# Kernel optimization log

Measured on AMD Instinct MI355X. Metric: run time of the kernel, lower is better.

Reference implementation:

```python
import jax, jax.numpy as jnp
import numpy as np
import math

NB_HEADS = 16
NUM_BUCKETS = 32
MAX_DISTANCE = 128


def _rel_bucket(qlen, klen, num_buckets=NUM_BUCKETS, max_distance=MAX_DISTANCE):
    # static (numpy) computation of T5 relative-position buckets, bidirectional
    relpos = np.arange(qlen)[:, None] - np.arange(klen)[None, :]
    n = -relpos
    nb = num_buckets // 2
    ret = (n < 0).astype(np.int64) * nb
    n = np.abs(n)
    max_exact = nb // 2
    is_small = n < max_exact
    val_if_large = max_exact + (
        np.log(np.maximum(n, 1) / max_exact) / math.log(max_distance / max_exact) * (nb - max_exact)
    ).astype(np.int64)
    val_if_large = np.minimum(val_if_large, nb - 1)
    return ret + np.where(is_small, n, val_if_large)


def _layer_normalize(x):
    # faithful to source: mean/biased-std over last dim, NO epsilon, no affine
    m = jnp.mean(x, axis=-1, keepdims=True)
    var = jnp.mean((x - m) ** 2, axis=-1, keepdims=True)
    return (x - m) / jnp.sqrt(var)


def setup_inputs() -> dict:
    key = jax.random.key(0)
    ks = jax.random.split(key, 16)
    B, L, D, F = 4, 1024, 1024, 4096
    s = 0.02
    inp = {
        "x": jax.random.normal(ks[0], (B, L, D), jnp.float32),
        "padding_mask": jnp.ones((B, L), jnp.int32),
        "Wq": jax.random.normal(ks[1], (D, D), jnp.float32) * s,
        "bq": jnp.zeros((D,), jnp.float32),
        "Wk": jax.random.normal(ks[2], (D, D), jnp.float32) * s,
        "bk": jnp.zeros((D,), jnp.float32),
        "Wv": jax.random.normal(ks[3], (D, D), jnp.float32) * s,
        "bv": jnp.zeros((D,), jnp.float32),
        "Wo": jax.random.normal(ks[4], (D, D), jnp.float32) * s,
        "bo": jnp.zeros((D,), jnp.float32),
        "rel_emb": jax.random.normal(ks[5], (NUM_BUCKETS, NB_HEADS), jnp.float32) * s,
        "W1": jax.random.normal(ks[6], (F, D), jnp.float32) * s,
        "b1": jnp.zeros((F,), jnp.float32),
        "W2": jax.random.normal(ks[7], (D, F), jnp.float32) * s,
        "b2": jnp.zeros((D,), jnp.float32),
    }
    return inp


def reference(x, padding_mask, Wq, bq, Wk, bk, Wv, bv, Wo, bo, rel_emb, W1, b1, W2, b2):
    B, L, D = x.shape
    H = NB_HEADS
    dh = D // H

    q = x @ Wq.T + bq
    k = x @ Wk.T + bk
    v = x @ Wv.T + bv

    # NOTE: source does a RAW reshape (B, L, H*dh) -> (B*H, L, dh); reproduce exactly
    qm = q.reshape(B * H, L, dh)
    km = k.reshape(B * H, L, dh)
    vm = v.reshape(B * H, L, dh)

    scores = jnp.einsum("bqd,bkd->bqk", qm, km)  # (B*H, L, L), no 1/sqrt(dh) scaling in source

    # relative position bias: emb[bucket] -> (L, L, H), tile heads B times, permute
    buckets = jnp.asarray(_rel_bucket(L, L))
    pos = rel_emb[buckets]                      # (L, L, H)
    bias = jnp.transpose(jnp.tile(pos, (1, 1, B)), (2, 0, 1))  # (H*B, L, L)
    scores = scores + bias

    # padding mask in log space, tiled exactly like source's repeat+view
    pm = jnp.log(padding_mask.astype(jnp.float32))            # (B, L)
    mask = jnp.tile(pm[:, None, :], (1, L, H)).reshape(-1, L, L)  # (B*H, L, L)
    scores = scores + mask

    p = jax.nn.softmax(scores, axis=-1)  # dropout is identity at p=0 / eval
    att = (p @ vm).reshape(B, L, D)
    att = att @ Wo.T + bo

    att_out = _layer_normalize(att + x)
    ff = jax.nn.relu(att_out @ W1.T + b1) @ W2.T + b2
    ff_out = _layer_normalize(ff + att_out)
    return ff_out
```

## Files before the change

### kernel.cpp

```cpp
#include <hip/hip_runtime.h>
#include <hip/hip_bf16.h>

typedef __hip_bfloat16 bf16;
typedef __attribute__((ext_vector_type(8))) short s8v;
typedef __attribute__((ext_vector_type(4))) float f32x4;

__device__ __forceinline__ float bits2f(unsigned short u) {
    return __uint_as_float(((unsigned)u) << 16);
}
__device__ __forceinline__ unsigned short f2b(float f) {
    union { float f; unsigned u; } x{f};
    return (unsigned short)((x.u + 0x7fff + ((x.u >> 16) & 1)) >> 16);
}
__device__ __forceinline__ float to_f(float x) { return x; }
__device__ __forceinline__ float to_f(unsigned short x) { return bits2f(x); }

__device__ __forceinline__ void load4(const float* p, float* a) {
    float4 t = *(const float4*)p;
    a[0] = t.x; a[1] = t.y; a[2] = t.z; a[3] = t.w;
}
__device__ __forceinline__ void load4(const unsigned short* p, float* a) {
    ushort4 t = *(const ushort4*)p;
    a[0] = bits2f(t.x); a[1] = bits2f(t.y); a[2] = bits2f(t.z); a[3] = bits2f(t.w);
}

__global__ __launch_bounds__(256)
void cvt_all_kernel(const float* __restrict__ x,
                    const float* __restrict__ Wq, const float* __restrict__ Wk,
                    const float* __restrict__ Wv, const float* __restrict__ Wo,
                    const float* __restrict__ W1, const float* __restrict__ W2,
                    unsigned short* __restrict__ xb, unsigned short* __restrict__ Wqkvb,
                    unsigned short* __restrict__ Wob,
                    unsigned short* __restrict__ W1b, unsigned short* __restrict__ W2b)
{
    int i = blockIdx.x * 256 + threadIdx.x;
    const float* src; unsigned short* dst; int off;
    if (i < (1 << 20))      { src = x;  dst = xb;  off = i; }
    else if (i < (2 << 20)) { src = W1; dst = W1b; off = i - (1 << 20); }
    else if (i < (3 << 20)) { src = W2; dst = W2b; off = i - (2 << 20); }
    else {
        int j = i - (3 << 20);
        int sel = j >> 18;
        off = j & ((1 << 18) - 1);
        src = sel == 0 ? Wq : sel == 1 ? Wk : sel == 2 ? Wv : Wo;
        dst = sel == 3 ? Wob : Wqkvb + ((size_t)sel << 20);
    }
    float4 v = ((const float4*)src)[off];
    ushort4 o = { f2b(v.x), f2b(v.y), f2b(v.z), f2b(v.w) };
    ((ushort4*)dst)[off] = o;
}

__global__ void rbias_kernel(const float* __restrict__ rel_emb, unsigned short* __restrict__ rbias)
{
    int idx = blockIdx.x * 256 + threadIdx.x;
    if (idx >= 16 * 2048) return;
    int h = idx >> 11, q = idx & 2047;
    int n = q - 1023, ret = 0;
    if (n < 0) { ret = 16; n = -n; }
    int b;
    if (n < 8) b = n;
    else {
        double t = log((double)n / 8.0) / log(16.0) * 8.0;
        int v = 8 + (int)t;
        b = v < 15 ? v : 15;
    }
    rbias[idx] = f2b(rel_emb[(ret + b) * 16 + h]);
}

template<typename TC, typename TR, int RELU, int QKV>
__global__ __launch_bounds__(256)
void mfma_gemm(const unsigned short* __restrict__ A, int lda,
               const unsigned short* __restrict__ W, int ldw,
               const float* __restrict__ b0, const float* __restrict__ b1,
               const float* __restrict__ b2,
               const TR* __restrict__ res,
               void* __restrict__ C0, void* __restrict__ C1, void* __restrict__ C2,
               int ldc, int M, int N, int Ksplit)
{
    __shared__ unsigned short sm[2 * 128 * 32];
    unsigned short* As = sm;
    unsigned short* Ws = sm + 128 * 32;

    const int tid = threadIdx.x;
    const int w = tid >> 6, lane = tid & 63;
    const int quad = lane >> 4, col = lane & 15;
    const int m0 = blockIdx.y * 128, n0 = blockIdx.x * 128;
    const int wrow = (w & 1) * 64, wcol = (w >> 1) * 64;
    const int kz = blockIdx.z * Ksplit;

    const int srow   = lane >> 2;
    const int schunk = (lane & 3) ^ ((lane >> 4) & 3);

    f32x4 acc[4][4] = {};

    for (int k0 = kz; k0 < kz + Ksplit; k0 += 32) {
        __syncthreads();
        #pragma unroll
        for (int t = 0; t < 2; ++t) {
            const int rbase = w * 32 + t * 16;
            unsigned off = (unsigned)(rbase * 64);
            off = __builtin_amdgcn_readfirstlane(off);
            const unsigned short* ga = A + (size_t)(m0 + rbase + srow) * lda + k0 + schunk * 8;
            __builtin_amdgcn_global_load_lds(
                (const __attribute__((address_space(1))) unsigned int*)ga,
                (__attribute__((address_space(3))) unsigned int*)((char*)As + off), 16, 0, 0);
            const unsigned short* gw = W + (size_t)(n0 + rbase + srow) * ldw + k0 + schunk * 8;
            __builtin_amdgcn_global_load_lds(
                (const __attribute__((address_space(1))) unsigned int*)gw,
                (__attribute__((address_space(3))) unsigned int*)((char*)Ws + off), 16, 0, 0);
        }
        __syncthreads();

        s8v af[4], bfr[4];
        #pragma unroll
        for (int mt = 0; mt < 4; ++mt) {
            int rr = wrow + mt * 16 + col;
            af[mt] = *(const s8v*)(As + rr * 32 + ((quad ^ ((rr >> 2) & 3)) * 8));
        }
        #pragma unroll
        for (int nt = 0; nt < 4; ++nt) {
            int rr = wcol + nt * 16 + col;
            bfr[nt] = *(const s8v*)(Ws + rr * 32 + ((quad ^ ((rr >> 2) & 3)) * 8));
        }
        #pragma unroll
        for (int mt = 0; mt < 4; ++mt)
            #pragma unroll
            for (int nt = 0; nt < 4; ++nt)
                acc[mt][nt] = __builtin_amdgcn_mfma_f32_16x16x32_bf16(af[mt], bfr[nt], acc[mt][nt], 0, 0, 0);
    }

    if (QKV) {
        const int sel = n0 >> 10;
        unsigned short* Cb = (unsigned short*)(sel == 0 ? C0 : sel == 1 ? C1 : C2);
        const float* bs = sel == 0 ? b0 : sel == 1 ? b1 : b2;
        #pragma unroll
        for (int mt = 0; mt < 4; ++mt)
            #pragma unroll
            for (int rg = 0; rg < 4; ++rg) {
                int gm = m0 + wrow + mt * 16 + quad * 4 + rg;
                #pragma unroll
                for (int nt = 0; nt < 4; ++nt) {
                    int gnc = (n0 + wcol + nt * 16 + col) & 1023;
                    Cb[(size_t)gm * 1024 + gnc] = f2b(acc[mt][nt][rg] + bs[gnc]);
                }
            }
    } else {
        void* Cv = blockIdx.z ? C1 : C0;
        const bool z0 = (blockIdx.z == 0);
        #pragma unroll
        for (int mt = 0; mt < 4; ++mt)
            #pragma unroll
            for (int rg = 0; rg < 4; ++rg) {
                int gm = m0 + wrow + mt * 16 + quad * 4 + rg;
                #pragma unroll
                for (int nt = 0; nt < 4; ++nt) {
                    int gn = n0 + wcol + nt * 16 + col;
                    float c = acc[mt][nt][rg];
                    if (z0) {
                        if (b0)  c += b0[gn];
                        if (res) c += to_f(res[(size_t)gm * ldc + gn]);
                    }
                    if (RELU) c = fmaxf(c, 0.f);
                    if (sizeof(TC) == 2) ((unsigned short*)Cv)[(size_t)gm * ldc + gn] = f2b(c);
                    else                 ((float*)Cv)[(size_t)gm * ldc + gn] = c;
                }
            }
    }
}


#define SWZ(r) ((((r) >> 2) & 3) | ((((r) >> 2) & 1) << 2))

__device__ __forceinline__ void stage_ht(const unsigned short* __restrict__ g, int ld,
                                         int grow0, int kbase,
                                         unsigned short* lds_half, int tid)
{
    #pragma unroll
    for (int l = 0; l < 2; ++l) {
        int idx = l * 512 + tid;
        int r = idx >> 3;
        int c = (idx & 7) ^ SWZ(r);
        const unsigned short* src = g + (size_t)(grow0 + r) * ld + kbase + c * 8;
        unsigned off = (unsigned)__builtin_amdgcn_readfirstlane((unsigned)((l * 512 + (tid & 448)) * 16));
        __builtin_amdgcn_global_load_lds(
            (const __attribute__((address_space(1))) unsigned int*)src,
            (__attribute__((address_space(3))) unsigned int*)((char*)lds_half + off), 16, 0, 0);
    }
}

#define PHASE(HM, HN, ...)                                                        \
    {                                                                             \
        __builtin_amdgcn_sched_barrier(0);                                        \
        s8v a_[4][2], b_[2][2];                                                   \
        _Pragma("unroll")                                                         \
        for (int mt2 = 0; mt2 < 4; ++mt2) {                                       \
            int r = ((HM) * 4 + mt2) * 32 + wm16 + col;                           \
            _Pragma("unroll")                                                     \
            for (int ks = 0; ks < 2; ++ks)                                        \
                a_[mt2][ks] = *(const s8v*)(dA + r * 64 + (((ks * 4 + quad) ^ SWZ(r)) << 3)); \
        }                                                                         \
        _Pragma("unroll")                                                         \
        for (int nt2 = 0; nt2 < 2; ++nt2) {                                       \
            int r = ((HN) * 2 + nt2) * 64 + wn16 + col;                           \
            _Pragma("unroll")                                                     \
            for (int ks = 0; ks < 2; ++ks)                                        \
                b_[nt2][ks] = *(const s8v*)(dB + r * 64 + (((ks * 4 + quad) ^ SWZ(r)) << 3)); \
        }                                                                         \
        __VA_ARGS__;                                                              \
        __builtin_amdgcn_sched_barrier(0);                                        \
        __builtin_amdgcn_s_barrier();                                             \
        asm volatile("s_waitcnt lgkmcnt(0)" ::: "memory");                        \
        __builtin_amdgcn_sched_barrier(0);                                        \
        __builtin_amdgcn_s_setprio(1);                                            \
        _Pragma("unroll")                                                         \
        for (int ks = 0; ks < 2; ++ks)                                            \
            _Pragma("unroll")                                                     \
            for (int mt2 = 0; mt2 < 4; ++mt2)                                     \
                _Pragma("unroll")                                                 \
                for (int nt2 = 0; nt2 < 2; ++nt2)                                 \
                    acc[(HM) * 4 + mt2][(HN) * 2 + nt2] =                         \
                        __builtin_amdgcn_mfma_f32_16x16x32_bf16(                  \
                            a_[mt2][ks], b_[nt2][ks], acc[(HM) * 4 + mt2][(HN) * 2 + nt2], 0, 0, 0); \
        __builtin_amdgcn_s_setprio(0);                                            \
        __builtin_amdgcn_sched_barrier(0);                                        \
    }

template<int MODE>
__global__ __launch_bounds__(512, 2)
void gemm256(const unsigned short* __restrict__ A, int lda,
             const unsigned short* __restrict__ W, int ldw,
             const float* __restrict__ bias0, const float* __restrict__ bias1,
             const float* __restrict__ bias2,
             const unsigned short* __restrict__ res,
             unsigned short* __restrict__ C0, unsigned short* __restrict__ C1,
             unsigned short* __restrict__ C2,
             int NT, int Ksplit)
{
    extern __shared__ unsigned short sm[];
    unsigned short* As0 = sm;
    unsigned short* Bs0 = sm + 32768;

    const int tid = threadIdx.x;
    const int w = tid >> 6, lane = tid & 63;
    const int quad = lane >> 4, col = lane & 15;
    const int wm16 = (w & 1) * 16, wn16 = (w >> 1) * 16;

    const int bid = blockIdx.x + gridDim.x * blockIdx.y;
    const int nwg = gridDim.x * gridDim.y;
    const int swz = (bid & 7) * (nwg >> 3) + (bid >> 3);
    const int m0 = (swz / gridDim.x) * 256;
    const int n0 = (swz % gridDim.x) * 256;
    const int kz = blockIdx.z * Ksplit;

    f32x4 acc[8][4] = {};

    stage_ht(A, lda, m0,       kz,      As0,                tid);
    stage_ht(W, ldw, n0,       kz,      Bs0,                tid);
    stage_ht(A, lda, m0 + 128, kz,      As0 + 8192,         tid);
    stage_ht(W, ldw, n0 + 128, kz,      Bs0 + 8192,         tid);
    stage_ht(A, lda, m0,       kz + 64, As0 + 16384,        tid);
    stage_ht(W, ldw, n0 + 128, kz + 64, Bs0 + 16384 + 8192, tid);
    asm volatile("s_waitcnt vmcnt(4)" ::: "memory");
    __builtin_amdgcn_sched_barrier(0);
    __builtin_amdgcn_s_barrier();

    for (int t = 0; t < NT; ++t) {
        const int cur = t & 1;
        const unsigned short* dA = As0 + cur * 16384;
        const unsigned short* dB = Bs0 + cur * 16384;
        unsigned short* Anx = As0 + (cur ^ 1) * 16384;
        unsigned short* Bnx = Bs0 + (cur ^ 1) * 16384;
        unsigned short* Acu = As0 + cur * 16384;
        unsigned short* Bcu = Bs0 + cur * 16384;
        const int k1 = kz + (t + 1) * 64, k2 = kz + (t + 2) * 64;
        const bool s1 = (t + 1 < NT), s2 = (t + 2 < NT);

        PHASE(0, 0, { if (s1) stage_ht(W, ldw, n0,       k1, Bnx,        tid); })
        __builtin_amdgcn_s_barrier();
        PHASE(0, 1, { if (s1) stage_ht(A, lda, m0 + 128, k1, Anx + 8192, tid); })
        __builtin_amdgcn_s_barrier();
        PHASE(1, 1, { if (s2) stage_ht(A, lda, m0,       k2, Acu,        tid); })
        __builtin_amdgcn_s_barrier();
        PHASE(1, 0, { if (s2) stage_ht(W, ldw, n0 + 128, k2, Bcu + 8192, tid); })
        if (s2) { asm volatile("s_waitcnt vmcnt(4)" ::: "memory"); }
        else    { asm volatile("s_waitcnt vmcnt(0)" ::: "memory"); }
        __builtin_amdgcn_sched_barrier(0);
        __builtin_amdgcn_s_barrier();
    }

    const int rb = m0 + wm16 + quad * 4;
    const int cb = wn16 + col;
    if (MODE == 0) {
        const int sel = n0 >> 10;
        unsigned short* Cb = sel == 0 ? C0 : sel == 1 ? C1 : C2;
        const float* bs = sel == 0 ? bias0 : sel == 1 ? bias1 : bias2;
        const int nb = (n0 & 1023) + cb;
        float bv[4];
        #pragma unroll
        for (int nt = 0; nt < 4; ++nt) bv[nt] = bs[nb + nt * 64];
        #pragma unroll
        for (int mt = 0; mt < 8; ++mt)
            #pragma unroll
            for (int rg = 0; rg < 4; ++rg) {
                const size_t ro = (size_t)(rb + mt * 32 + rg) * 1024 + nb;
                #pragma unroll
                for (int nt = 0; nt < 4; ++nt)
                    Cb[ro + nt * 64] = f2b(acc[mt][nt][rg] + bv[nt]);
            }
    } else if (MODE == 1) {
        float bv[4];
        #pragma unroll
        for (int nt = 0; nt < 4; ++nt) bv[nt] = bias0[n0 + cb + nt * 64];
        #pragma unroll
        for (int mt = 0; mt < 8; ++mt)
            #pragma unroll
            for (int rg = 0; rg < 4; ++rg) {
                const size_t ro = (size_t)(rb + mt * 32 + rg) * 4096 + n0 + cb;
                #pragma unroll
                for (int nt = 0; nt < 4; ++nt)
                    C0[ro + nt * 64] = f2b(fmaxf(acc[mt][nt][rg] + bv[nt], 0.f));
            }
    } else {
        unsigned short* Cb = blockIdx.z ? C1 : C0;
        const bool z0 = (blockIdx.z == 0);
        float bv[4];
        #pragma unroll
        for (int nt = 0; nt < 4; ++nt) bv[nt] = z0 ? bias0[n0 + cb + nt * 64] : 0.f;
        #pragma unroll
        for (int mt = 0; mt < 8; ++mt)
            #pragma unroll
            for (int rg = 0; rg < 4; ++rg) {
                const size_t ro = (size_t)(rb + mt * 32 + rg) * 1024 + n0 + cb;
                #pragma unroll
                for (int nt = 0; nt < 4; ++nt) {
                    float c = acc[mt][nt][rg] + bv[nt];
                    if (z0) c += bits2f(res[ro + nt * 64]);
                    Cb[ro + nt * 64] = f2b(c);
                }
            }
    }
}

__global__ __launch_bounds__(256)
void vtrans_kernel(const unsigned short* __restrict__ v, unsigned short* __restrict__ vt)
{
    __shared__ unsigned short t[64][68];
    const int bpmm = blockIdx.x;
    const int bp = bpmm >> 6, mm = bpmm & 63;
    const unsigned short* vr = v + (size_t)(bp * 64 + mm) * 1024;
    const int tid = threadIdx.x;
    #pragma unroll
    for (int it = 0; it < 4; ++it) {
        int c = (tid >> 6) + it * 4;
        int d = tid & 63;
        t[d][c] = vr[c * 64 + d];
    }
    __syncthreads();
    int d = tid >> 2, qq = tid & 3;
    ushort4 o = { t[d][qq * 4 + 0], t[d][qq * 4 + 1], t[d][qq * 4 + 2], t[d][qq * 4 + 3] };
    *(ushort4*)(vt + (size_t)bp * 65536 + (size_t)d * 1024 + mm * 16 + qq * 4) = o;
}

__global__ __launch_bounds__(256, 2)
void attn_mfma_kernel(const unsigned short* __restrict__ qb,
                      const unsigned short* __restrict__ kb,
                      const unsigned short* __restrict__ vt,
                      const unsigned short* __restrict__ rbias,
                      const int* __restrict__ pmask,
                      unsigned short* __restrict__ att)
{
    __shared__ unsigned short Qs[128 * 64];
    __shared__ unsigned short KP[128 * 64];
    __shared__ unsigned short Vt[64 * 128];
    __shared__ unsigned short rbs[2048];
    __shared__ unsigned short pmls[1024];

    const int tid = threadIdx.x;
    const int w = tid >> 6, lane = tid & 63;
    const int quad = lane >> 4, col = lane & 15;
    const int bp = blockIdx.x, i0 = blockIdx.y * 128;
    const int h = bp & 15, bb = bp >> 4;
    const size_t base = (size_t)bp << 16;
    const int myrow0 = w * 32, myrow1 = w * 32 + 16;

    {
        const unsigned short* qg = qb + base + (size_t)i0 * 64;
        #pragma unroll
        for (int it = 0; it < 4; ++it) {
            int idx = it * 256 + tid;
            int r = idx >> 3, c = idx & 7;
            s8v d = *(const s8v*)(qg + (size_t)r * 64 + (c ^ (r & 7)) * 8);
            *(s8v*)(Qs + r * 64 + c * 8) = d;
        }
    }
    {
        const unsigned short* rg = rbias + h * 2048;
        #pragma unroll
        for (int it = 0; it < 8; ++it) rbs[it * 256 + tid] = rg[it * 256 + tid];
    }
    #pragma unroll
    for (int it = 0; it < 4; ++it) {
        int j = it * 256 + tid;
        pmls[j] = f2b(__logf((float)pmask[bb * 1024 + j]));
    }

    f32x4 O0[4] = {}, O1[4] = {};
    float lrow0[4] = {0.f, 0.f, 0.f, 0.f};
    float lrow1[4] = {0.f, 0.f, 0.f, 0.f};

    unsigned short* Pw = KP + w * 2048;

    for (int jt = 0; jt < 8; ++jt) {
        const int j0 = jt * 128;
        __syncthreads();
        {
            const unsigned short* kg = kb + base + (size_t)j0 * 64;
            #pragma unroll
            for (int it = 0; it < 4; ++it) {
                int idx = it * 256 + tid;
                int r = idx >> 3, c = idx & 7;
                s8v d = *(const s8v*)(kg + (size_t)r * 64 + (c ^ (r & 7)) * 8);
                *(s8v*)(KP + r * 64 + c * 8) = d;
            }
            const unsigned short* vg = vt + base + j0;
            #pragma unroll
            for (int it = 0; it < 4; ++it) {
                int idx = it * 256 + tid;
                int r = idx >> 4, c = idx & 15;
                s8v d = *(const s8v*)(vg + (size_t)r * 1024 + (c ^ (r & 15)) * 8);
                *(s8v*)(Vt + r * 128 + c * 8) = d;
            }
        }
        __syncthreads();

        f32x4 S0[8] = {}, S1[8] = {};
        #pragma unroll
        for (int ks = 0; ks < 2; ++ks) {
            int ar0 = myrow0 + col, ar1 = myrow1 + col;
            s8v a0 = *(const s8v*)(Qs + ar0 * 64 + (((ks * 4 + quad) ^ (ar0 & 7)) * 8));
            s8v a1 = *(const s8v*)(Qs + ar1 * 64 + (((ks * 4 + quad) ^ (ar1 & 7)) * 8));
            #pragma unroll
            for (int ct = 0; ct < 8; ++ct) {
                int br = ct * 16 + col;
                s8v b = *(const s8v*)(KP + br * 64 + (((ks * 4 + quad) ^ (br & 7)) * 8));
                S0[ct] = __builtin_amdgcn_mfma_f32_16x16x32_bf16(a0, b, S0[ct], 0, 0, 0);
                S1[ct] = __builtin_amdgcn_mfma_f32_16x16x32_bf16(a1, b, S1[ct], 0, 0, 0);
            }
        }

        #pragma unroll
        for (int ct = 0; ct < 8; ++ct) {
            int gj = j0 + ct * 16 + col;
            float pmv = bits2f(pmls[gj]);
            int d0 = gj - (i0 + myrow0 + quad * 4) + 1023;
            int d1 = gj - (i0 + myrow1 + quad * 4) + 1023;
            #pragma unroll
            for (int r = 0; r < 4; ++r) {
                float e0 = __expf(S0[ct][r] + bits2f(rbs[d0 - r]) + pmv);
                float e1 = __expf(S1[ct][r] + bits2f(rbs[d1 - r]) + pmv);
                S0[ct][r] = e0; lrow0[r] += e0;
                S1[ct][r] = e1; lrow1[r] += e1;
            }
        }

        __syncthreads();

        #pragma unroll
        for (int ct = 0; ct < 8; ++ct)
            #pragma unroll
            for (int r = 0; r < 4; ++r) {
                int lr = quad * 4 + r;
                int j = ct * 16 + col;
                Pw[lr * 128 + (((j >> 3) ^ lr) << 3) + (j & 7)] = f2b(S0[ct][r]);
            }
        #pragma unroll
        for (int kt = 0; kt < 4; ++kt) {
            int pr = col;
            s8v a = *(const s8v*)(Pw + pr * 128 + (((kt * 4 + quad) ^ pr) * 8));
            #pragma unroll
            for (int nt = 0; nt < 4; ++nt) {
                int vr = nt * 16 + col;
                s8v b = *(const s8v*)(Vt + vr * 128 + (((kt * 4 + quad) ^ (vr & 15)) * 8));
                O0[nt] = __builtin_amdgcn_mfma_f32_16x16x32_bf16(a, b, O0[nt], 0, 0, 0);
            }
        }

        #pragma unroll
        for (int ct = 0; ct < 8; ++ct)
            #pragma unroll
            for (int r = 0; r < 4; ++r) {
                int lr = quad * 4 + r;
                int j = ct * 16 + col;
                Pw[lr * 128 + (((j >> 3) ^ lr) << 3) + (j & 7)] = f2b(S1[ct][r]);
            }
        #pragma unroll
        for (int kt = 0; kt < 4; ++kt) {
            int pr = col;
            s8v a = *(const s8v*)(Pw + pr * 128 + (((kt * 4 + quad) ^ pr) * 8));
            #pragma unroll
            for (int nt = 0; nt < 4; ++nt) {
                int vr = nt * 16 + col;
                s8v b = *(const s8v*)(Vt + vr * 128 + (((kt * 4 + quad) ^ (vr & 15)) * 8));
                O1[nt] = __builtin_amdgcn_mfma_f32_16x16x32_bf16(a, b, O1[nt], 0, 0, 0);
            }
        }
    }

    #pragma unroll
    for (int off = 1; off < 16; off <<= 1)
        #pragma unroll
        for (int r = 0; r < 4; ++r) {
            lrow0[r] += __shfl_xor(lrow0[r], off);
            lrow1[r] += __shfl_xor(lrow1[r], off);
        }
    #pragma unroll
    for (int r = 0; r < 4; ++r) {
        lrow0[r] = 1.f / lrow0[r];
        lrow1[r] = 1.f / lrow1[r];
    }

    unsigned short* ag0 = att + base + (size_t)(i0 + myrow0) * 64;
    unsigned short* ag1 = att + base + (size_t)(i0 + myrow1) * 64;
    #pragma unroll
    for (int nt = 0; nt < 4; ++nt)
        #pragma unroll
        for (int r = 0; r < 4; ++r) {
            ag0[(size_t)(quad * 4 + r) * 64 + nt * 16 + col] = f2b(O0[nt][r] * lrow0[r]);
            ag1[(size_t)(quad * 4 + r) * 64 + nt * 16 + col] = f2b(O1[nt][r] * lrow1[r]);
        }
}

template<typename TIN>
__global__ __launch_bounds__(256)
void ln_kernel(const TIN* __restrict__ in1, const TIN* __restrict__ in2,
               float* __restrict__ outF, unsigned short* __restrict__ outB)
{
    __shared__ float sred[8];
    const int row = blockIdx.x;
    const int tid = threadIdx.x;
    const size_t off = (size_t)row * 1024 + tid * 4;
    float a[4];
    load4(in1 + off, a);
    if (in2) {
        float b[4];
        load4(in2 + off, b);
        #pragma unroll
        for (int i = 0; i < 4; ++i) a[i] += b[i];
    }

    float lsum = a[0] + a[1] + a[2] + a[3];
    #pragma unroll
    for (int o = 32; o; o >>= 1) lsum += __shfl_down(lsum, o);
    const int lane = tid & 63, wid = tid >> 6;
    if (lane == 0) sred[wid] = lsum;
    __syncthreads();
    if (tid == 0) sred[4] = (sred[0] + sred[1] + sred[2] + sred[3]) * (1.f / 1024.f);
    __syncthreads();
    const float mean = sred[4];

    float d0 = a[0] - mean, d1 = a[1] - mean, d2 = a[2] - mean, d3 = a[3] - mean;
    float lsq = d0 * d0 + d1 * d1 + d2 * d2 + d3 * d3;
    #pragma unroll
    for (int o = 32; o; o >>= 1) lsq += __shfl_down(lsq, o);
    __syncthreads();
    if (lane == 0) sred[wid] = lsq;
    __syncthreads();
    if (tid == 0) sred[5] = rsqrtf((sred[0] + sred[1] + sred[2] + sred[3]) * (1.f / 1024.f));
    __syncthreads();
    const float r = sred[5];

    float o0 = d0 * r, o1 = d1 * r, o2 = d2 * r, o3 = d3 * r;
    if (outF) {
        float4 o = {o0, o1, o2, o3};
        *(float4*)&outF[off] = o;
    }
    if (outB) {
        ushort4 o = { f2b(o0), f2b(o1), f2b(o2), f2b(o3) };
        *(ushort4*)&outB[off] = o;
    }
}

extern "C" void kernel_launch(void* const* d_in, const int* in_sizes, int n_in,
                              void* d_out, int out_size, void* d_ws, size_t ws_size,
                              hipStream_t stream)
{
    const float* x     = (const float*)d_in[0];
    const int*   pmask = (const int*)  d_in[1];
    const float* Wq    = (const float*)d_in[2];
    const float* bq    = (const float*)d_in[3];
    const float* Wk    = (const float*)d_in[4];
    const float* bk    = (const float*)d_in[5];
    const float* Wv    = (const float*)d_in[6];
    const float* bv    = (const float*)d_in[7];
    const float* Wo    = (const float*)d_in[8];
    const float* bo    = (const float*)d_in[9];
    const float* rel   = (const float*)d_in[10];
    const float* W1    = (const float*)d_in[11];
    const float* b1    = (const float*)d_in[12];
    const float* W2    = (const float*)d_in[13];
    const float* b2    = (const float*)d_in[14];

    const int M = 4096, D = 1024;
    dim3 blk(256);

    char* ws = (char*)d_ws;
    unsigned short* W1b   = (unsigned short*)(ws);
    unsigned short* W2b   = (unsigned short*)(ws + ( 8u << 20));
    unsigned short* xb    = (unsigned short*)(ws + (16u << 20));
    unsigned short* Wqkvb = (unsigned short*)(ws + (24u << 20));
    unsigned short* Wob   = (unsigned short*)(ws + (30u << 20));
    unsigned short* qb    = (unsigned short*)(ws + (32u << 20));
    unsigned short* kb    = (unsigned short*)(ws + (40u << 20));
    unsigned short* vb    = (unsigned short*)(ws + (48u << 20));
    unsigned short* vt    = (unsigned short*)(ws + (56u << 20));
    unsigned short* rbias = (unsigned short*)(ws + (64u << 20));
    float*          tmpA    = (float*)(ws + (32u << 20));
    float*          tmpB    = (float*)(ws + (48u << 20));
    unsigned short* attoutB = (unsigned short*)(ws + (16u << 20));
    unsigned short* ff1     = (unsigned short*)(ws + (32u << 20));
    unsigned short* ff2a    = (unsigned short*)(ws);
    unsigned short* ff2b    = (unsigned short*)(ws + (24u << 20));
    unsigned short* attb    = (unsigned short*)d_out;

    static bool attrset = false;
    if (!attrset) {
        hipFuncSetAttribute(reinterpret_cast<const void*>(gemm256<0>),
                            hipFuncAttributeMaxDynamicSharedMemorySize, 131072);
        hipFuncSetAttribute(reinterpret_cast<const void*>(gemm256<1>),
                            hipFuncAttributeMaxDynamicSharedMemorySize, 131072);
        hipFuncSetAttribute(reinterpret_cast<const void*>(gemm256<2>),
                            hipFuncAttributeMaxDynamicSharedMemorySize, 131072);
        attrset = true;
    }

    cvt_all_kernel<<<16384, blk, 0, stream>>>(x, Wq, Wk, Wv, Wo, W1, W2,
                                              xb, Wqkvb, Wob, W1b, W2b);
    rbias_kernel<<<128, blk, 0, stream>>>(rel, rbias);

    gemm256<0><<<dim3(12, 16), dim3(512), 131072, stream>>>(
        xb, D, Wqkvb, D, bq, bk, bv, nullptr, qb, kb, vb, 16, 0);

    vtrans_kernel<<<4096, blk, 0, stream>>>(vb, vt);

    attn_mfma_kernel<<<dim3(64, 8), blk, 0, stream>>>(qb, kb, vt, rbias, pmask, attb);

    mfma_gemm<float, float, 0, 0><<<dim3(8, 32, 2), blk, 0, stream>>>(
        attb, D, Wob, D, bo, nullptr, nullptr, x, tmpA, tmpB, nullptr, D, M, D, 512);
    ln_kernel<float><<<4096, blk, 0, stream>>>(tmpA, tmpB, nullptr, attoutB);

    gemm256<1><<<dim3(16, 16), dim3(512), 131072, stream>>>(
        attoutB, D, W1b, D, b1, nullptr, nullptr, nullptr, ff1, nullptr, nullptr, 16, 0);
    gemm256<2><<<dim3(4, 16, 2), dim3(512), 131072, stream>>>(
        ff1, 4096, W2b, 4096, b2, nullptr, nullptr, attoutB, ff2a, ff2b, nullptr, 32, 2048);
    ln_kernel<unsigned short><<<4096, blk, 0, stream>>>(ff2a, ff2b, (float*)d_out, nullptr);
}
```

Measured before the change: 463.1 us.

## Reorder GEMM quadrant schedule to reuse A/B fragments and change LDS swizzle

Restructures the 256x256 GEMM main loop so register fragments are reused across quadrants in the order (0,0),(1,0),(1,1),(0,1). Each phase now reloads only one of the A or B fragment sets instead of both, which cuts LDS reads. The prefetch order and the vmcnt waits are changed to match, and the LDS XOR swizzle becomes a plain r&7. The removed sched_barriers and lgkmcnt waits leave the compiler to order LDS reads against the MFMAs, which could cause stalls or hazards.

```diff
diff --git a/kernel.cpp b/kernel.cpp
--- a/kernel.cpp
+++ b/kernel.cpp
@@ -169,8 +169,6 @@
 }
 
 
-#define SWZ(r) ((((r) >> 2) & 3) | ((((r) >> 2) & 1) << 2))
-
 __device__ __forceinline__ void stage_ht(const unsigned short* __restrict__ g, int ld,
                                          int grow0, int kbase,
                                          unsigned short* lds_half, int tid)
@@ -179,7 +177,7 @@
     for (int l = 0; l < 2; ++l) {
         int idx = l * 512 + tid;
         int r = idx >> 3;
-        int c = (idx & 7) ^ SWZ(r);
+        int c = (idx & 7) ^ (r & 7);
         const unsigned short* src = g + (size_t)(grow0 + r) * ld + kbase + c * 8;
         unsigned off = (unsigned)__builtin_amdgcn_readfirstlane((unsigned)((l * 512 + (tid & 448)) * 16));
         __builtin_amdgcn_global_load_lds(
@@ -188,42 +186,36 @@
     }
 }
 
-#define PHASE(HM, HN, ...)                                                        \
-    {                                                                             \
-        __builtin_amdgcn_sched_barrier(0);                                        \
-        s8v a_[4][2], b_[2][2];                                                   \
-        _Pragma("unroll")                                                         \
-        for (int mt2 = 0; mt2 < 4; ++mt2) {                                       \
-            int r = ((HM) * 4 + mt2) * 32 + wm16 + col;                           \
-            _Pragma("unroll")                                                     \
-            for (int ks = 0; ks < 2; ++ks)                                        \
-                a_[mt2][ks] = *(const s8v*)(dA + r * 64 + (((ks * 4 + quad) ^ SWZ(r)) << 3)); \
-        }                                                                         \
-        _Pragma("unroll")                                                         \
-        for (int nt2 = 0; nt2 < 2; ++nt2) {                                       \
-            int r = ((HN) * 2 + nt2) * 64 + wn16 + col;                           \
-            _Pragma("unroll")                                                     \
-            for (int ks = 0; ks < 2; ++ks)                                        \
-                b_[nt2][ks] = *(const s8v*)(dB + r * 64 + (((ks * 4 + quad) ^ SWZ(r)) << 3)); \
-        }                                                                         \
-        __VA_ARGS__;                                                              \
-        __builtin_amdgcn_sched_barrier(0);                                        \
-        __builtin_amdgcn_s_barrier();                                             \
-        asm volatile("s_waitcnt lgkmcnt(0)" ::: "memory");                        \
-        __builtin_amdgcn_sched_barrier(0);                                        \
-        __builtin_amdgcn_s_setprio(1);                                            \
+#define LDA(HM)                                                                   \
+    _Pragma("unroll")                                                             \
+    for (int mt2 = 0; mt2 < 4; ++mt2) {                                           \
+        int r = ((HM) * 4 + mt2) * 32 + wm16 + col;                               \
         _Pragma("unroll")                                                         \
         for (int ks = 0; ks < 2; ++ks)                                            \
+            aA[mt2][ks] = *(const s8v*)(dA + r * 64 + (((ks * 4 + quad) ^ (r & 7)) << 3)); \
+    }
+
+#define LDB(HN)                                                                   \
+    _Pragma("unroll")                                                             \
+    for (int nt2 = 0; nt2 < 2; ++nt2) {                                           \
+        int r = ((HN) * 2 + nt2) * 64 + wn16 + col;                               \
+        _Pragma("unroll")                                                         \
+        for (int ks = 0; ks < 2; ++ks)                                            \
+            bB[nt2][ks] = *(const s8v*)(dB + r * 64 + (((ks * 4 + quad) ^ (r & 7)) << 3)); \
+    }
+
+#define MFMAQ(HM, HN)                                                             \
+    __builtin_amdgcn_s_setprio(1);                                                \
+    _Pragma("unroll")                                                             \
+    for (int ks = 0; ks < 2; ++ks)                                                \
+        _Pragma("unroll")                                                         \
+        for (int mt2 = 0; mt2 < 4; ++mt2)                                         \
             _Pragma("unroll")                                                     \
-            for (int mt2 = 0; mt2 < 4; ++mt2)                                     \
-                _Pragma("unroll")                                                 \
-                for (int nt2 = 0; nt2 < 2; ++nt2)                                 \
-                    acc[(HM) * 4 + mt2][(HN) * 2 + nt2] =                         \
-                        __builtin_amdgcn_mfma_f32_16x16x32_bf16(                  \
-                            a_[mt2][ks], b_[nt2][ks], acc[(HM) * 4 + mt2][(HN) * 2 + nt2], 0, 0, 0); \
-        __builtin_amdgcn_s_setprio(0);                                            \
-        __builtin_amdgcn_sched_barrier(0);                                        \
-    }
+            for (int nt2 = 0; nt2 < 2; ++nt2)                                     \
+                acc[(HM) * 4 + mt2][(HN) * 2 + nt2] =                             \
+                    __builtin_amdgcn_mfma_f32_16x16x32_bf16(                      \
+                        aA[mt2][ks], bB[nt2][ks], acc[(HM) * 4 + mt2][(HN) * 2 + nt2], 0, 0, 0); \
+    __builtin_amdgcn_s_setprio(0);
 
 template<int MODE>
 __global__ __launch_bounds__(512, 2)
@@ -254,37 +246,54 @@
 
     f32x4 acc[8][4] = {};
 
-    stage_ht(A, lda, m0,       kz,      As0,                tid);
     stage_ht(W, ldw, n0,       kz,      Bs0,                tid);
     stage_ht(A, lda, m0 + 128, kz,      As0 + 8192,         tid);
+    stage_ht(A, lda, m0,       kz,      As0,                tid);
     stage_ht(W, ldw, n0 + 128, kz,      Bs0 + 8192,         tid);
-    stage_ht(A, lda, m0,       kz + 64, As0 + 16384,        tid);
-    stage_ht(W, ldw, n0 + 128, kz + 64, Bs0 + 16384 + 8192, tid);
-    asm volatile("s_waitcnt vmcnt(4)" ::: "memory");
-    __builtin_amdgcn_sched_barrier(0);
+    stage_ht(W, ldw, n0,       kz + 64, Bs0 + 16384,        tid);
+    stage_ht(A, lda, m0 + 128, kz + 64, As0 + 16384 + 8192, tid);
+    asm volatile("s_waitcnt vmcnt(6)" ::: "memory");
     __builtin_amdgcn_s_barrier();
 
     for (int t = 0; t < NT; ++t) {
         const int cur = t & 1;
         const unsigned short* dA = As0 + cur * 16384;
         const unsigned short* dB = Bs0 + cur * 16384;
-        unsigned short* Anx = As0 + (cur ^ 1) * 16384;
-        unsigned short* Bnx = Bs0 + (cur ^ 1) * 16384;
-        unsigned short* Acu = As0 + cur * 16384;
-        unsigned short* Bcu = Bs0 + cur * 16384;
+        unsigned short* nA = As0 + (cur ^ 1) * 16384;
+        unsigned short* nB = Bs0 + (cur ^ 1) * 16384;
+        unsigned short* cA = (unsigned short*)dA;
+        unsigned short* cB = (unsigned short*)dB;
         const int k1 = kz + (t + 1) * 64, k2 = kz + (t + 2) * 64;
         const bool s1 = (t + 1 < NT), s2 = (t + 2 < NT);
 
-        PHASE(0, 0, { if (s1) stage_ht(W, ldw, n0,       k1, Bnx,        tid); })
-        __builtin_amdgcn_s_barrier();
-        PHASE(0, 1, { if (s1) stage_ht(A, lda, m0 + 128, k1, Anx + 8192, tid); })
-        __builtin_amdgcn_s_barrier();
-        PHASE(1, 1, { if (s2) stage_ht(A, lda, m0,       k2, Acu,        tid); })
-        __builtin_amdgcn_s_barrier();
-        PHASE(1, 0, { if (s2) stage_ht(W, ldw, n0 + 128, k2, Bcu + 8192, tid); })
-        if (s2) { asm volatile("s_waitcnt vmcnt(4)" ::: "memory"); }
+        s8v aA[4][2], bB[2][2];
+
+        LDA(0); LDB(0);
+        if (s1) stage_ht(A, lda, m0, k1, nA, tid);
+        __builtin_amdgcn_s_barrier();
+        MFMAQ(0, 0);
+        __builtin_amdgcn_s_barrier();
+
+        LDA(1);
+        if (s1) stage_ht(W, ldw, n0 + 128, k1, nB + 8192, tid);
+        __builtin_amdgcn_s_barrier();
+        MFMAQ(1, 0);
+        if (s2) { asm volatile("s_waitcnt vmcnt(8)" ::: "memory"); }
         else    { asm volatile("s_waitcnt vmcnt(0)" ::: "memory"); }
-        __builtin_amdgcn_sched_barrier(0);
+        __builtin_amdgcn_s_barrier();
+
+        LDB(1);
+        if (s2) stage_ht(W, ldw, n0, k2, cB, tid);
+        __builtin_amdgcn_s_barrier();
+        MFMAQ(1, 1);
+        __builtin_amdgcn_s_barrier();
+
+        LDA(0);
+        if (s2) stage_ht(A, lda, m0 + 128, k2, cA + 8192, tid);
+        __builtin_amdgcn_s_barrier();
+        MFMAQ(0, 1);
+        if (s2) { asm volatile("s_waitcnt vmcnt(6)" ::: "memory"); }
+        else    { asm volatile("s_waitcnt vmcnt(0)" ::: "memory"); }
         __builtin_amdgcn_s_barrier();
     }
 
```

Result: faster. 420.2 us (-9.3%).
